# Optimization experiments

Hardware: AMD Instinct MI355X
Metric: run time of the kernel (lower is better)

The kernel has to match this reference:

```python
import jax, jax.numpy as jnp
import numpy as np


def _lc2d(x, W, b, kh, kw):
    """Locally connected conv: distinct (Cout,Cin,kh,kw) kernel per output location.
    x: [B,Cin,H,W]; W: [Hout,Wout,Cout,Cin,kh,kw]; b: [Hout,Wout,Cout].
    Kernel size == stride, so each output pixel sees a disjoint kh x kw patch."""
    B, C, H, Wd = x.shape
    Hout, Wout = H // kh, Wd // kw
    patches = x.reshape(B, C, Hout, kh, Wout, kw)  # [b,c,i,k,j,l]
    out = jnp.einsum('bcikjl,ijockl->boij', patches, W)
    return out + b.transpose(2, 0, 1)[None]  # [B,Cout,Hout,Wout]


def setup_inputs() -> dict:
    key = jax.random.key(0)
    ks = jax.random.split(key, 11)

    def u(k, shape, fan_in):
        bound = 1.0 / np.sqrt(fan_in)
        return jax.random.uniform(k, shape, jnp.float32, -bound, bound)

    B = 4096
    x = jax.random.normal(ks[0], (B, 6, 60, 60), jnp.float32)
    info = jax.random.normal(ks[1], (B, 2), jnp.float32)
    # b0: 20x20 locations, Conv2d(6->32, 3x3)
    W0 = u(ks[2], (20, 20, 32, 6, 3, 3), 6 * 9)
    B0 = u(ks[3], (20, 20, 32), 6 * 9)
    # b1: 10x10 locations, Conv2d(32->64, 2x2)
    W1 = u(ks[4], (10, 10, 64, 32, 2, 2), 32 * 4)
    B1 = u(ks[5], (10, 10, 64), 32 * 4)
    # b2: 2x2 locations, Conv2d(64->128, 5x5)
    W2 = u(ks[6], (2, 2, 128, 64, 5, 5), 64 * 25)
    B2 = u(ks[7], (2, 2, 128), 64 * 25)
    # classifier Linear(514, 2); stored as [in, out]
    Wc = u(ks[8], (514, 2), 514)
    bc = u(ks[9], (2,), 514)
    return {"x": x, "info": info, "W0": W0, "B0": B0, "W1": W1, "B1": B1,
            "W2": W2, "B2": B2, "Wc": Wc, "bc": bc}


def reference(x, info, W0, B0, W1, B1, W2, B2, Wc, bc):
    h = jnp.tanh(_lc2d(x, W0, B0, 3, 3))   # [B,32,20,20]
    h = jnp.tanh(_lc2d(h, W1, B1, 2, 2))   # [B,64,10,10]
    h = jnp.tanh(_lc2d(h, W2, B2, 5, 5))   # [B,128,2,2]
    h = h.reshape(h.shape[0], -1)          # [B,512]
    h = jnp.concatenate([h, info], axis=1)  # [B,514]
    logits = h @ Wc + bc                    # [B,2]
    return jax.nn.softmax(logits, axis=1)
```

## Files before the change

kernel.cpp:

```cpp
#include <hip/hip_runtime.h>

typedef short short8 __attribute__((ext_vector_type(8)));
typedef float floatx4 __attribute__((ext_vector_type(4)));

__device__ __forceinline__ unsigned short f2bf(float f) {
  union { float f; unsigned int i; } v; v.f = f;
  return (unsigned short)((v.i + 0x7fffu + ((v.i >> 16) & 1u)) >> 16);
}
__device__ __forceinline__ float ftanh(float x) {
  float e = __expf(2.f * x);
  return 1.f - 2.f / (e + 1.f);
}

__global__ __launch_bounds__(256) void k_permute(const float* __restrict__ W0,
                                                 const float* __restrict__ W1,
                                                 const float* __restrict__ W2,
                                                 unsigned short* __restrict__ W0f,
                                                 unsigned short* __restrict__ W1f,
                                                 unsigned short* __restrict__ W2f) {
  int idx = blockIdx.x * 256 + threadIdx.x;
  int sec = idx / 819200;
  int q = idx - sec * 819200;
  int frag = q >> 9, li = q & 511;
  int lane = li >> 3, e = li & 7;
  int n = lane & 15, quad = lane >> 4;
  if (sec == 0) {
    int loc = frag >> 2, nt = (frag >> 1) & 1, ks = frag & 1;
    int kk = (ks << 5) + (quad << 3) + e;
    int co = (nt << 4) + n;
    unsigned short v = 0;
    if (kk < 54) v = f2bf(W0[loc * 1728 + co * 54 + kk]);
    W0f[q] = v;
  } else if (sec == 1) {
    int loc = frag >> 4, nt = (frag >> 2) & 3, ks = frag & 3;
    int kk = (ks << 5) + (quad << 3) + e;
    int kl = kk >> 5, c = kk & 31, co = (nt << 4) + n;
    W1f[q] = f2bf(W1[(size_t)loc * 8192 + (co << 7) + (c << 2) + kl]);
  } else {
    int g = frag / 50, ks = frag - g * 50;
    int loc = g >> 3, nt = g & 7;
    int kk = (ks << 5) + (quad << 3) + e;
    int kl5 = kk >> 6, c = kk & 63, co = (nt << 4) + n;
    W2f[q] = f2bf(W2[(size_t)loc * 204800 + co * 1600 + c * 25 + kl5]);
  }
}

__global__ __launch_bounds__(320, 5) void k_l0(const float* __restrict__ x,
                                               const short8* __restrict__ W0f,
                                               const float* __restrict__ B0,
                                               unsigned short* __restrict__ h0) {
  const int t = threadIdx.x;
  const int b0 = blockIdx.x << 4;
  const int i = blockIdx.y;
  __shared__ __align__(16) unsigned short sX[16 * 1128];

  {
    const int b = t / 20, j = t - (t / 20) * 20;
    const float* xb = x + (size_t)(b0 + b) * 21600 + (3 * i) * 60 + 3 * j;
    unsigned short* dst = &sX[b * 1128 + j * 56];
    int c = 0, r = 0;
#pragma unroll
    for (int p = 0; p < 9; ++p) {
      const float* pa = xb + c * 3600 + r * 60;
      float a0 = pa[0], a1 = pa[1], a2 = pa[2];
      ++r; if (r == 3) { r = 0; ++c; }
      const float* pb = xb + c * 3600 + r * 60;
      float b0v = pb[0], b1v = pb[1], b2v = pb[2];
      ++r; if (r == 3) { r = 0; ++c; }
      unsigned int w0 = (unsigned int)f2bf(a0) | ((unsigned int)f2bf(a1) << 16);
      unsigned int w1 = (unsigned int)f2bf(a2) | ((unsigned int)f2bf(b0v) << 16);
      unsigned int w2 = (unsigned int)f2bf(b1v) | ((unsigned int)f2bf(b2v) << 16);
      *(unsigned int*)&dst[p * 6]     = w0;
      *(unsigned int*)&dst[p * 6 + 2] = w1;
      *(unsigned int*)&dst[p * 6 + 4] = w2;
    }
    *(unsigned int*)&dst[54] = 0u;
  }
  __syncthreads();

  const int lane = t & 63, w = t >> 6;
  const int n16 = lane & 15, quad = lane >> 4;
  const floatx4 z = {0.f, 0.f, 0.f, 0.f};

#pragma unroll
  for (int jj = 0; jj < 4; ++jj) {
    const int j = (w << 2) + jj;
    const int loc = i * 20 + j;
    short8 a0 = *(const short8*)&sX[n16 * 1128 + j * 56 + (quad << 3)];
    short8 a1 = {};
    if (quad < 3) a1 = *(const short8*)&sX[n16 * 1128 + j * 56 + 32 + (quad << 3)];

    short8 b00 = W0f[((loc << 2) + 0) * 64 + lane];
    short8 b01 = W0f[((loc << 2) + 1) * 64 + lane];
    short8 b10 = W0f[((loc << 2) + 2) * 64 + lane];
    short8 b11 = W0f[((loc << 2) + 3) * 64 + lane];

    floatx4 acc0 = z, acc1 = z;
    acc0 = __builtin_amdgcn_mfma_f32_16x16x32_bf16(a0, b00, acc0, 0, 0, 0);
    acc0 = __builtin_amdgcn_mfma_f32_16x16x32_bf16(a1, b01, acc0, 0, 0, 0);
    acc1 = __builtin_amdgcn_mfma_f32_16x16x32_bf16(a0, b10, acc1, 0, 0, 0);
    acc1 = __builtin_amdgcn_mfma_f32_16x16x32_bf16(a1, b11, acc1, 0, 0, 0);

    const int o_off = (((i >> 1) * 10 + (j >> 1)) << 7) + (((i & 1) * 2 + (j & 1)) << 5);
    float bias0 = B0[loc * 32 + n16];
    float bias1 = B0[loc * 32 + 16 + n16];
#pragma unroll
    for (int reg = 0; reg < 4; ++reg) {
      int bb = b0 + (quad << 2) + reg;
      h0[(size_t)bb * 12800 + o_off + n16]      = f2bf(ftanh(acc0[reg] + bias0));
      h0[(size_t)bb * 12800 + o_off + 16 + n16] = f2bf(ftanh(acc1[reg] + bias1));
    }
  }
}

__global__ __launch_bounds__(256, 2) void k_l12(const unsigned short* __restrict__ h0,
                                                const short8* __restrict__ W1f,
                                                const float* __restrict__ B1,
                                                const short8* __restrict__ W2f,
                                                const float* __restrict__ B2,
                                                float* __restrict__ h2) {
  const int t = threadIdx.x, lane = t & 63, w = t >> 6;
  const int n16 = lane & 15, quad = lane >> 4;
  const int b0 = blockIdx.x << 4;
  const int q = blockIdx.y;
  const int i0 = (q >> 1) * 5, j0 = (q & 1) * 5;

  __shared__ __align__(16) unsigned short sH[16 * 1608];

  const floatx4 z = {0.f, 0.f, 0.f, 0.f};

  for (int li = w; li < 25; li += 4) {
    const int di = li / 5, dj = li - di * 5;
    const int loc = (i0 + di) * 10 + (j0 + dj);

    short8 a[4];
#pragma unroll
    for (int ks = 0; ks < 4; ++ks)
      a[ks] = *(const short8*)&h0[(size_t)(b0 + n16) * 12800 + (loc << 7) + (ks << 5) + (quad << 3)];

    floatx4 acc[4] = {z, z, z, z};
#pragma unroll
    for (int ks = 0; ks < 4; ++ks)
#pragma unroll
      for (int nt = 0; nt < 4; ++nt)
        acc[nt] = __builtin_amdgcn_mfma_f32_16x16x32_bf16(
            a[ks], W1f[(((loc << 2) + nt) << 2) * 64 + ks * 64 + lane], acc[nt], 0, 0, 0);

#pragma unroll
    for (int nt = 0; nt < 4; ++nt) {
      float bias = B1[(loc << 6) + (nt << 4) + n16];
      int col = (li << 6) + (nt << 4) + n16;
#pragma unroll
      for (int reg = 0; reg < 4; ++reg)
        sH[((quad << 2) + reg) * 1608 + col] = f2bf(ftanh(acc[nt][reg] + bias));
    }
  }
  __syncthreads();

  floatx4 acc0 = z, acc1 = z;
  const short8* wb0 = W2f + (size_t)(((q << 3) + (w << 1)) * 50) * 64 + lane;
  const short8* wb1 = wb0 + (size_t)50 * 64;
  for (int ks = 0; ks < 50; ++ks) {
    short8 a = *(const short8*)&sH[n16 * 1608 + (ks << 5) + (quad << 3)];
    acc0 = __builtin_amdgcn_mfma_f32_16x16x32_bf16(a, wb0[ks * 64], acc0, 0, 0, 0);
    acc1 = __builtin_amdgcn_mfma_f32_16x16x32_bf16(a, wb1[ks * 64], acc1, 0, 0, 0);
  }

#pragma unroll
  for (int u = 0; u < 2; ++u) {
    const floatx4& ac = u ? acc1 : acc0;
    int co = (((w << 1) + u) << 4) + n16;
    float bias = B2[(q << 7) + co];
#pragma unroll
    for (int reg = 0; reg < 4; ++reg) {
      int bb = b0 + (quad << 2) + reg;
      h2[(size_t)bb * 512 + (co << 2) + q] = ftanh(ac[reg] + bias);
    }
  }
}

__global__ __launch_bounds__(256) void k_cls(const float* __restrict__ h2,
                                             const float* __restrict__ info,
                                             const float* __restrict__ Wc,
                                             const float* __restrict__ bc,
                                             float* __restrict__ out) {
  const int l = threadIdx.x & 63;
  const int b = blockIdx.x * 4 + (threadIdx.x >> 6);
  const float* hrow = h2 + (size_t)b * 512;
  float p0 = 0.f, p1 = 0.f;
#pragma unroll
  for (int f = 0; f < 512; f += 64) {
    float h = hrow[f + l];
    p0 = fmaf(h, Wc[2 * (f + l)], p0);
    p1 = fmaf(h, Wc[2 * (f + l) + 1], p1);
  }
#pragma unroll
  for (int m = 32; m; m >>= 1) {
    p0 += __shfl_xor(p0, m, 64);
    p1 += __shfl_xor(p1, m, 64);
  }
  if (l == 0) {
    float i0 = info[2 * b], i1 = info[2 * b + 1];
    float l0 = p0 + i0 * Wc[1024] + i1 * Wc[1026] + bc[0];
    float l1 = p1 + i0 * Wc[1025] + i1 * Wc[1027] + bc[1];
    float mx = fmaxf(l0, l1);
    float e0 = __expf(l0 - mx), e1 = __expf(l1 - mx);
    float inv = 1.f / (e0 + e1);
    out[2 * b]     = e0 * inv;
    out[2 * b + 1] = e1 * inv;
  }
}

extern "C" void kernel_launch(void* const* d_in, const int* in_sizes, int n_in,
                              void* d_out, int out_size, void* d_ws, size_t ws_size,
                              hipStream_t stream) {
  const float* x    = (const float*)d_in[0];
  const float* info = (const float*)d_in[1];
  const float* W0   = (const float*)d_in[2];
  const float* B0   = (const float*)d_in[3];
  const float* W1   = (const float*)d_in[4];
  const float* B1   = (const float*)d_in[5];
  const float* W2   = (const float*)d_in[6];
  const float* B2   = (const float*)d_in[7];
  const float* Wc   = (const float*)d_in[8];
  const float* bc   = (const float*)d_in[9];
  float* out = (float*)d_out;

  char* ws = (char*)d_ws;
  unsigned short* h0  = (unsigned short*)ws;
  float*          h2  = (float*)(ws + 104857600);
  unsigned short* W0f = (unsigned short*)(ws + 113246208);
  unsigned short* W1f = (unsigned short*)(ws + 114884608);
  unsigned short* W2f = (unsigned short*)(ws + 116523008);

  k_permute<<<dim3(9600),    dim3(256), 0, stream>>>(W0, W1, W2, W0f, W1f, W2f);
  k_l0     <<<dim3(256, 20), dim3(320), 0, stream>>>(x, (const short8*)W0f, B0, h0);
  k_l12    <<<dim3(256, 4),  dim3(256), 0, stream>>>(h0, (const short8*)W1f, B1,
                                                     (const short8*)W2f, B2, h2);
  k_cls    <<<dim3(1024),    dim3(256), 0, stream>>>(h2, info, Wc, bc, out);
}
```

Baseline: 597.1 us.

## Fuse layer 0 into layer 1/2 kernel, dropping the h0 global round-trip

Merges the first locally-connected layer into the fused layer-1/2 kernel, so each block stages its 6x6 input patches from x into LDS and computes the 2x2 layer-0 outputs on chip instead of writing and re-reading a ~100MB bf16 h0 buffer. The next patch is staged while layer-1 MFMAs run, and layer 1 is split by output tile across warps. This removes heavy global memory traffic but adds two block-wide barriers per location over 25 serial iterations, and input loads become scattered float2 reads.

```diff
diff --git a/kernel.cpp b/kernel.cpp
--- a/kernel.cpp
+++ b/kernel.cpp
@@ -45,117 +45,107 @@
   }
 }
 
-__global__ __launch_bounds__(320, 5) void k_l0(const float* __restrict__ x,
-                                               const short8* __restrict__ W0f,
-                                               const float* __restrict__ B0,
-                                               unsigned short* __restrict__ h0) {
-  const int t = threadIdx.x;
-  const int b0 = blockIdx.x << 4;
-  const int i = blockIdx.y;
-  __shared__ __align__(16) unsigned short sX[16 * 1128];
-
-  {
-    const int b = t / 20, j = t - (t / 20) * 20;
-    const float* xb = x + (size_t)(b0 + b) * 21600 + (3 * i) * 60 + 3 * j;
-    unsigned short* dst = &sX[b * 1128 + j * 56];
-    int c = 0, r = 0;
-#pragma unroll
-    for (int p = 0; p < 9; ++p) {
-      const float* pa = xb + c * 3600 + r * 60;
-      float a0 = pa[0], a1 = pa[1], a2 = pa[2];
-      ++r; if (r == 3) { r = 0; ++c; }
-      const float* pb = xb + c * 3600 + r * 60;
-      float b0v = pb[0], b1v = pb[1], b2v = pb[2];
-      ++r; if (r == 3) { r = 0; ++c; }
-      unsigned int w0 = (unsigned int)f2bf(a0) | ((unsigned int)f2bf(a1) << 16);
-      unsigned int w1 = (unsigned int)f2bf(a2) | ((unsigned int)f2bf(b0v) << 16);
-      unsigned int w2 = (unsigned int)f2bf(b1v) | ((unsigned int)f2bf(b2v) << 16);
-      *(unsigned int*)&dst[p * 6]     = w0;
-      *(unsigned int*)&dst[p * 6 + 2] = w1;
-      *(unsigned int*)&dst[p * 6 + 4] = w2;
-    }
-    *(unsigned int*)&dst[54] = 0u;
-  }
-  __syncthreads();
-
-  const int lane = t & 63, w = t >> 6;
-  const int n16 = lane & 15, quad = lane >> 4;
-  const floatx4 z = {0.f, 0.f, 0.f, 0.f};
-
-#pragma unroll
-  for (int jj = 0; jj < 4; ++jj) {
-    const int j = (w << 2) + jj;
-    const int loc = i * 20 + j;
-    short8 a0 = *(const short8*)&sX[n16 * 1128 + j * 56 + (quad << 3)];
-    short8 a1 = {};
-    if (quad < 3) a1 = *(const short8*)&sX[n16 * 1128 + j * 56 + 32 + (quad << 3)];
-
-    short8 b00 = W0f[((loc << 2) + 0) * 64 + lane];
-    short8 b01 = W0f[((loc << 2) + 1) * 64 + lane];
-    short8 b10 = W0f[((loc << 2) + 2) * 64 + lane];
-    short8 b11 = W0f[((loc << 2) + 3) * 64 + lane];
-
-    floatx4 acc0 = z, acc1 = z;
-    acc0 = __builtin_amdgcn_mfma_f32_16x16x32_bf16(a0, b00, acc0, 0, 0, 0);
-    acc0 = __builtin_amdgcn_mfma_f32_16x16x32_bf16(a1, b01, acc0, 0, 0, 0);
-    acc1 = __builtin_amdgcn_mfma_f32_16x16x32_bf16(a0, b10, acc1, 0, 0, 0);
-    acc1 = __builtin_amdgcn_mfma_f32_16x16x32_bf16(a1, b11, acc1, 0, 0, 0);
-
-    const int o_off = (((i >> 1) * 10 + (j >> 1)) << 7) + (((i & 1) * 2 + (j & 1)) << 5);
-    float bias0 = B0[loc * 32 + n16];
-    float bias1 = B0[loc * 32 + 16 + n16];
-#pragma unroll
-    for (int reg = 0; reg < 4; ++reg) {
-      int bb = b0 + (quad << 2) + reg;
-      h0[(size_t)bb * 12800 + o_off + n16]      = f2bf(ftanh(acc0[reg] + bias0));
-      h0[(size_t)bb * 12800 + o_off + 16 + n16] = f2bf(ftanh(acc1[reg] + bias1));
-    }
-  }
-}
-
-__global__ __launch_bounds__(256, 2) void k_l12(const unsigned short* __restrict__ h0,
-                                                const short8* __restrict__ W1f,
-                                                const float* __restrict__ B1,
-                                                const short8* __restrict__ W2f,
-                                                const float* __restrict__ B2,
-                                                float* __restrict__ h2) {
+__global__ __launch_bounds__(256, 2) void k_fused(const float* __restrict__ x,
+                                                  const short8* __restrict__ W0f,
+                                                  const float* __restrict__ B0,
+                                                  const short8* __restrict__ W1f,
+                                                  const float* __restrict__ B1,
+                                                  const short8* __restrict__ W2f,
+                                                  const float* __restrict__ B2,
+                                                  float* __restrict__ h2) {
   const int t = threadIdx.x, lane = t & 63, w = t >> 6;
   const int n16 = lane & 15, quad = lane >> 4;
-  const int b0 = blockIdx.x << 4;
-  const int q = blockIdx.y;
+  const int q = blockIdx.x;
+  const int b0 = blockIdx.y << 4;
   const int i0 = (q >> 1) * 5, j0 = (q & 1) * 5;
 
+  __shared__ __align__(16) unsigned short sX[16 * 264];
+  __shared__ __align__(16) unsigned short sA[16 * 136];
   __shared__ __align__(16) unsigned short sH[16 * 1608];
 
   const floatx4 z = {0.f, 0.f, 0.f, 0.f};
-
-  for (int li = w; li < 25; li += 4) {
+  const float* xq = x + (size_t)b0 * 21600;
+
+  if (t < 64) {
+    unsigned int* d = (unsigned int*)&sX[(t >> 2) * 264 + (t & 3) * 64 + 54];
+    d[0] = 0u; d[1] = 0u; d[2] = 0u; d[3] = 0u; d[4] = 0u;
+  }
+
+  auto stage = [&](int gi, int gj) {
+    const float* base = xq + gi * 360 + gj * 6;
+#pragma unroll
+    for (int uu = 0; uu < 3; ++uu) {
+      int u = t + (uu << 8);
+      if (uu == 2 && t >= 64) continue;
+      int b = u / 36, rem = u - b * 36;
+      int c = rem / 6, rr = rem - c * 6;
+      const float2* p = (const float2*)(base + (size_t)b * 21600 + c * 3600 + rr * 60);
+      float2 v0 = p[0], v1 = p[1], v2 = p[2];
+      int si = (rr >= 3) ? 1 : 0, r = rr - si * 3;
+      unsigned short* d0 = &sX[b * 264 + (si << 1) * 64 + c * 9 + r * 3];
+      d0[0]  = f2bf(v0.x); d0[1]  = f2bf(v0.y); d0[2]  = f2bf(v1.x);
+      d0[64] = f2bf(v1.y); d0[65] = f2bf(v2.x); d0[66] = f2bf(v2.y);
+    }
+  };
+
+  stage(i0, j0);
+  __syncthreads();
+
+  for (int li = 0; li < 25; ++li) {
     const int di = li / 5, dj = li - di * 5;
-    const int loc = (i0 + di) * 10 + (j0 + dj);
-
-    short8 a[4];
-#pragma unroll
-    for (int ks = 0; ks < 4; ++ks)
-      a[ks] = *(const short8*)&h0[(size_t)(b0 + n16) * 12800 + (loc << 7) + (ks << 5) + (quad << 3)];
-
-    floatx4 acc[4] = {z, z, z, z};
-#pragma unroll
-    for (int ks = 0; ks < 4; ++ks)
-#pragma unroll
-      for (int nt = 0; nt < 4; ++nt)
-        acc[nt] = __builtin_amdgcn_mfma_f32_16x16x32_bf16(
-            a[ks], W1f[(((loc << 2) + nt) << 2) * 64 + ks * 64 + lane], acc[nt], 0, 0, 0);
-
-#pragma unroll
-    for (int nt = 0; nt < 4; ++nt) {
-      float bias = B1[(loc << 6) + (nt << 4) + n16];
-      int col = (li << 6) + (nt << 4) + n16;
+    const int gi = i0 + di, gj = j0 + dj;
+
+    {
+      const int s = w;
+      const int loc0 = (2 * gi + (s >> 1)) * 20 + (2 * gj + (s & 1));
+      short8 a0 = *(const short8*)&sX[n16 * 264 + s * 64 + (quad << 3)];
+      short8 a1 = *(const short8*)&sX[n16 * 264 + s * 64 + 32 + (quad << 3)];
+      short8 b00 = W0f[((loc0 << 2) + 0) * 64 + lane];
+      short8 b01 = W0f[((loc0 << 2) + 1) * 64 + lane];
+      short8 b10 = W0f[((loc0 << 2) + 2) * 64 + lane];
+      short8 b11 = W0f[((loc0 << 2) + 3) * 64 + lane];
+      floatx4 acc0 = z, acc1 = z;
+      acc0 = __builtin_amdgcn_mfma_f32_16x16x32_bf16(a0, b00, acc0, 0, 0, 0);
+      acc0 = __builtin_amdgcn_mfma_f32_16x16x32_bf16(a1, b01, acc0, 0, 0, 0);
+      acc1 = __builtin_amdgcn_mfma_f32_16x16x32_bf16(a0, b10, acc1, 0, 0, 0);
+      acc1 = __builtin_amdgcn_mfma_f32_16x16x32_bf16(a1, b11, acc1, 0, 0, 0);
+      float bias0 = B0[loc0 * 32 + n16];
+      float bias1 = B0[loc0 * 32 + 16 + n16];
+#pragma unroll
+      for (int reg = 0; reg < 4; ++reg) {
+        unsigned short* dd = &sA[((quad << 2) + reg) * 136 + (s << 5) + n16];
+        dd[0]  = f2bf(ftanh(acc0[reg] + bias0));
+        dd[16] = f2bf(ftanh(acc1[reg] + bias1));
+      }
+    }
+    __syncthreads();
+
+    if (li < 24) {
+      const int lin = li + 1;
+      const int din = lin / 5, djn = lin - din * 5;
+      stage(i0 + din, j0 + djn);
+    }
+
+    {
+      const int loc1 = gi * 10 + gj;
+      short8 a0 = *(const short8*)&sA[n16 * 136 + 0  + (quad << 3)];
+      short8 a1 = *(const short8*)&sA[n16 * 136 + 32 + (quad << 3)];
+      short8 a2 = *(const short8*)&sA[n16 * 136 + 64 + (quad << 3)];
+      short8 a3 = *(const short8*)&sA[n16 * 136 + 96 + (quad << 3)];
+      const short8* wb = W1f + (size_t)(((loc1 << 2) + w) << 2) * 64 + lane;
+      floatx4 acc = z;
+      acc = __builtin_amdgcn_mfma_f32_16x16x32_bf16(a0, wb[0],   acc, 0, 0, 0);
+      acc = __builtin_amdgcn_mfma_f32_16x16x32_bf16(a1, wb[64],  acc, 0, 0, 0);
+      acc = __builtin_amdgcn_mfma_f32_16x16x32_bf16(a2, wb[128], acc, 0, 0, 0);
+      acc = __builtin_amdgcn_mfma_f32_16x16x32_bf16(a3, wb[192], acc, 0, 0, 0);
+      float bias = B1[(loc1 << 6) + (w << 4) + n16];
+      int col = (li << 6) + (w << 4) + n16;
 #pragma unroll
       for (int reg = 0; reg < 4; ++reg)
-        sH[((quad << 2) + reg) * 1608 + col] = f2bf(ftanh(acc[nt][reg] + bias));
-    }
-  }
-  __syncthreads();
+        sH[((quad << 2) + reg) * 1608 + col] = f2bf(ftanh(acc[reg] + bias));
+    }
+    __syncthreads();
+  }
 
   floatx4 acc0 = z, acc1 = z;
   const short8* wb0 = W2f + (size_t)(((q << 3) + (w << 1)) * 50) * 64 + lane;
@@ -227,15 +217,14 @@
   float* out = (float*)d_out;
 
   char* ws = (char*)d_ws;
-  unsigned short* h0  = (unsigned short*)ws;
-  float*          h2  = (float*)(ws + 104857600);
-  unsigned short* W0f = (unsigned short*)(ws + 113246208);
-  unsigned short* W1f = (unsigned short*)(ws + 114884608);
-  unsigned short* W2f = (unsigned short*)(ws + 116523008);
+  float*          h2  = (float*)ws;
+  unsigned short* W0f = (unsigned short*)(ws + 8388608);
+  unsigned short* W1f = (unsigned short*)(ws + 10027008);
+  unsigned short* W2f = (unsigned short*)(ws + 11665408);
 
   k_permute<<<dim3(9600),    dim3(256), 0, stream>>>(W0, W1, W2, W0f, W1f, W2f);
-  k_l0     <<<dim3(256, 20), dim3(320), 0, stream>>>(x, (const short8*)W0f, B0, h0);
-  k_l12    <<<dim3(256, 4),  dim3(256), 0, stream>>>(h0, (const short8*)W1f, B1,
+  k_fused  <<<dim3(4, 256),  dim3(256), 0, stream>>>(x, (const short8*)W0f, B0,
+                                                     (const short8*)W1f, B1,
                                                      (const short8*)W2f, B2, h2);
   k_cls    <<<dim3(1024),    dim3(256), 0, stream>>>(h2, info, Wc, bc, out);
 }
```

New measurement: 697.6 us. 1.17x slower.
